# Kernel tuning notes

Hardware: AMD Instinct MI355X
Metric: run time of the kernel (lower is better)

## Reference

```python
import jax, jax.numpy as jnp
import numpy as np

EPS = 1e-5

def _patches(x, k, stride, pad):
    # x: [B, C, H, W] -> [B, L, C*k*k] with patch features ordered (c, kh, kw)
    # matching torch unfold / adder2d weight layout [Cout, Cin, kh, kw].
    B, C, H, W = x.shape
    xp = jnp.pad(x, ((0, 0), (0, 0), (pad, pad), (pad, pad)))
    Ho = (H + 2 * pad - k) // stride + 1
    Wo = (W + 2 * pad - k) // stride + 1
    cols = [xp[:, :, i:i + stride * Ho:stride, j:j + stride * Wo:stride]
            for i in range(k) for j in range(k)]
    p = jnp.stack(cols, axis=2)                      # [B, C, k*k, Ho, Wo]
    p = p.reshape(B, C * k * k, Ho * Wo)             # [B, K, L]
    return p.transpose(0, 2, 1), Ho, Wo              # [B, L, K]


def adder2d(x, w, stride, pad):
    # AdderNet layer: out[n,co,h,w] = -sum_{ci,kh,kw} |x_patch - w[co]|
    B = x.shape[0]
    Cout, Cin, k, _ = w.shape
    P, Ho, Wo = _patches(x, k, stride, pad)          # [B, L, K]
    Wf = w.reshape(Cout, Cin * k * k)                # [Cout, K]

    @jax.checkpoint
    def per_out(wrow):                               # wrow: [K]
        return -jnp.sum(jnp.abs(P - wrow), axis=-1)  # [B, L]

    out = jax.lax.map(per_out, Wf)                   # [Cout, B, L]
    return out.transpose(1, 0, 2).reshape(B, Cout, Ho, Wo)


def batchnorm(x, gamma, beta):
    # training-mode BatchNorm2d: batch statistics over (N, H, W)
    mu = jnp.mean(x, axis=(0, 2, 3), keepdims=True)
    var = jnp.var(x, axis=(0, 2, 3), keepdims=True)
    xn = (x - mu) * jax.lax.rsqrt(var + EPS)
    return xn * gamma[None, :, None, None] + beta[None, :, None, None]


def setup_inputs() -> dict:
    key = jax.random.key(0)
    kx, kw1, kw2 = jax.random.split(key, 3)
    B, C, H, W = 32, 64, 32, 32
    return {
        "x": jax.random.normal(kx, (B, C, H, W), dtype=jnp.float32),
        "w1": jax.random.normal(kw1, (C, C, 3, 3), dtype=jnp.float32),
        "g1": jnp.ones((C,), dtype=jnp.float32),
        "b1": jnp.zeros((C,), dtype=jnp.float32),
        "w2": jax.random.normal(kw2, (C, C, 3, 3), dtype=jnp.float32),
        "g2": jnp.ones((C,), dtype=jnp.float32),
        "b2": jnp.zeros((C,), dtype=jnp.float32),
    }


def reference(x, w1, g1, b1, w2, g2, b2):
    out = adder2d(x, w1, stride=1, pad=1)
    out = jax.nn.relu(batchnorm(out, g1, b1))
    out = adder2d(out, w2, stride=1, pad=1)
    out = batchnorm(out, g2, b2)
    return jax.nn.relu(out + x)
```

## Files before the change

### kernel.cpp

```cpp
#include <hip/hip_runtime.h>

#define CH    64
#define HWHW  1024
#define CHW   65536
#define NPIX  32768.0f

#define QS16   4096.0f
#define QB16   32768.5f
#define Q0P    0x80008000u
#define QINV16 2.44140625e-4f

#define PLSTRIDE 496
#define ROWSTR   51
#define NPLANES  4096

#define AS1 __attribute__((address_space(1)))
#define AS3 __attribute__((address_space(3)))

__device__ __forceinline__ unsigned q16(float x) {
  unsigned u = (unsigned)fmaf(x, QS16, QB16);
  return u > 65535u ? 65535u : u;
}
__device__ __forceinline__ unsigned q16pk(float lo, float hi) {
  return q16(lo) | (q16(hi) << 16);
}

__device__ __forceinline__ unsigned sad16(unsigned x, unsigned w, unsigned a) {
  unsigned d;
  asm("v_sad_u16 %0, %1, %2, %3" : "=v"(d) : "v"(x), "v"(w), "v"(a));
  return d;
}

__device__ __forceinline__ void gll16(const unsigned* g, unsigned* l) {
  __builtin_amdgcn_global_load_lds((const AS1 unsigned*)g, (AS3 unsigned*)l, 16, 0, 0);
}

__global__ __launch_bounds__(256) void prep_kernel(
    const float* __restrict__ w1, const float* __restrict__ w2,
    unsigned* __restrict__ wt1, unsigned* __restrict__ wt2,
    float* __restrict__ stats) {
  int j = blockIdx.x * 256 + threadIdx.x;
  if (j < 256) stats[j] = 0.0f;
  if (j < 18432) {
    int colo = j & 3;
    int t = j >> 2;
    int kw = t % 3; t /= 3;
    int kh = t % 3; t /= 3;
    int cp = t & 7; t >>= 3;
    int wv = t & 3; int cog = t >> 2;
    int co  = cog * 4 + colo;
    int cil = wv * 16 + cp * 2;
    int slo = co * 576 + cil * 9 + kh * 3 + kw;
    wt1[j] = q16pk(w1[slo], w1[slo + 9]);
    wt2[j] = q16pk(w2[slo], w2[slo + 9]);
  }
}

__global__ __launch_bounds__(256) void qx_kernel(
    const float* __restrict__ x, unsigned* __restrict__ xq) {
  int idx = blockIdx.x * 256 + threadIdx.x;
  if (idx >= NPLANES * PLSTRIDE) return;
  int pl = idx / PLSTRIDE;
  int j  = idx - pl * PLSTRIDE;
  int p  = pl & 31;
  int rg = (pl >> 5) & 3;
  int n  = pl >> 7;
  int row = j / ROWSTR;
  int ci  = j - row * ROWSTR;
  int col = ci - 1;
  int hr  = rg * 8 - 1 + row;
  unsigned v = Q0P;
  if (ci >= 1 && ci <= 32 && hr >= 0 && hr < 32) {
    const float* px = x + n * CHW + (2 * p) * HWHW + hr * 32 + col;
    v = q16pk(px[0], px[HWHW]);
  }
  xq[idx] = v;
}

__global__ __launch_bounds__(256) void bnq_kernel(
    const float* __restrict__ A, const float* __restrict__ stats,
    const float* __restrict__ g, const float* __restrict__ b,
    unsigned* __restrict__ xq) {
  int idx = blockIdx.x * 256 + threadIdx.x;
  if (idx >= NPLANES * PLSTRIDE) return;
  int pl = idx / PLSTRIDE;
  int j  = idx - pl * PLSTRIDE;
  int p  = pl & 31;
  int rg = (pl >> 5) & 3;
  int n  = pl >> 7;
  int row = j / ROWSTR;
  int ci  = j - row * ROWSTR;
  int col = ci - 1;
  int hr  = rg * 8 - 1 + row;
  unsigned v = Q0P;
  if (ci >= 1 && ci <= 32 && hr >= 0 && hr < 32) {
    int ch0 = 2 * p, ch1 = 2 * p + 1;
    float mu0 = stats[ch0] * (1.0f / NPIX);
    float va0 = fmaf(-mu0, mu0, stats[64 + ch0] * (1.0f / NPIX));
    float rs0 = rsqrtf(va0 + 1e-5f);
    float ga0 = g[ch0] * rs0;
    float be0 = fmaf(-mu0, ga0, b[ch0]);
    float mu1 = stats[ch1] * (1.0f / NPIX);
    float va1 = fmaf(-mu1, mu1, stats[64 + ch1] * (1.0f / NPIX));
    float rs1 = rsqrtf(va1 + 1e-5f);
    float ga1 = g[ch1] * rs1;
    float be1 = fmaf(-mu1, ga1, b[ch1]);
    float v0 = fmaxf(fmaf(A[n * CHW + ch0 * HWHW + hr * 32 + col], ga0, be0), 0.0f);
    float v1 = fmaxf(fmaf(A[n * CHW + ch1 * HWHW + hr * 32 + col], ga1, be1), 0.0f);
    v = q16pk(v0, v1);
  }
  xq[idx] = v;
}

__global__ __launch_bounds__(256, 6) void adder_kernel(
    const unsigned* __restrict__ xq,
    const unsigned* __restrict__ wt,
    float* __restrict__ out,
    float* __restrict__ stats) {
  const int cog  = blockIdx.x;
  const int rg   = blockIdx.y;
  const int n    = blockIdx.z;
  const int tid  = threadIdx.x;
  const int lane = tid & 63;
  const int wv   = __builtin_amdgcn_readfirstlane(tid >> 6);
  const int co0  = cog * 4;
  const int r0   = lane >> 3;
  const int c0   = (lane & 7) * 4;

  __shared__ __align__(16) unsigned lds[5120];
  unsigned* buf0 = lds + wv * 992;
  unsigned* buf1 = buf0 + 496;
  unsigned* wl   = lds + 3968;
  unsigned* red  = lds;

  const char* gpb = (const char*)(xq + (((n * 4 + rg) * 32) + wv * 8) * PLSTRIDE);
  const int lane16 = lane * 16;

  gll16((const unsigned*)(gpb + lane16), buf0);
  gll16((const unsigned*)(gpb + 960 + lane16), buf0 + 240);
  {
    const uint4* wsrc = (const uint4*)(wt + cog * 1152);
    for (int i = tid; i < 288; i += 256) ((uint4*)wl)[i] = wsrc[i];
  }
  __syncthreads();

  unsigned acc[4][4];
#pragma unroll
  for (int co = 0; co < 4; ++co)
#pragma unroll
    for (int j = 0; j < 4; ++j) acc[co][j] = 0u;

#pragma unroll
  for (int cp = 0; cp < 8; ++cp) {
    if (cp < 7) {
      unsigned* nbuf = (cp & 1) ? buf0 : buf1;
      const char* s = gpb + (cp + 1) * (PLSTRIDE * 4);
      gll16((const unsigned*)(s + lane16), nbuf);
      gll16((const unsigned*)(s + 960 + lane16), nbuf + 240);
      asm volatile("s_waitcnt vmcnt(2)" ::: "memory");
    } else {
      asm volatile("s_waitcnt vmcnt(0)" ::: "memory");
    }
    const unsigned* cbuf = (cp & 1) ? buf1 : buf0;
    const unsigned* wpb = wl + wv * 288 + cp * 36;
#pragma unroll
    for (int kh = 0; kh < 3; ++kh) {
      const uint4* wp = (const uint4*)(wpb + kh * 12);
      uint4 wa = wp[0], wb = wp[1], wc = wp[2];
      unsigned w[12] = {wa.x, wa.y, wa.z, wa.w, wb.x, wb.y, wb.z, wb.w,
                        wc.x, wc.y, wc.z, wc.w};
      const unsigned* rp = cbuf + (r0 + kh) * ROWSTR + c0;
      unsigned xv[6];
#pragma unroll
      for (int j = 0; j < 6; ++j) xv[j] = rp[j];
#pragma unroll
      for (int kw = 0; kw < 3; ++kw)
#pragma unroll
        for (int co = 0; co < 4; ++co) {
          unsigned ww = w[kw * 4 + co];
          acc[co][0] = sad16(xv[kw + 0], ww, acc[co][0]);
          acc[co][1] = sad16(xv[kw + 1], ww, acc[co][1]);
          acc[co][2] = sad16(xv[kw + 2], ww, acc[co][2]);
          acc[co][3] = sad16(xv[kw + 3], ww, acc[co][3]);
        }
    }
  }

  __syncthreads();
  if (wv != 0) {
    unsigned* rp = red + (wv - 1) * 1280 + lane * 20;
#pragma unroll
    for (int co = 0; co < 4; ++co) {
      uint4 q = {acc[co][0], acc[co][1], acc[co][2], acc[co][3]};
      *(uint4*)(rp + co * 4) = q;
    }
  }
  __syncthreads();

  if (wv == 0) {
#pragma unroll
    for (int s = 0; s < 3; ++s) {
      const unsigned* rp = red + s * 1280 + lane * 20;
#pragma unroll
      for (int co = 0; co < 4; ++co) {
        uint4 q = *(const uint4*)(rp + co * 4);
        acc[co][0] += q.x; acc[co][1] += q.y; acc[co][2] += q.z; acc[co][3] += q.w;
      }
    }
    const int ob = n * CHW + (rg * 8 + r0) * 32 + c0;
#pragma unroll
    for (int co = 0; co < 4; ++co) {
      float t0 = -(float)acc[co][0] * QINV16;
      float t1 = -(float)acc[co][1] * QINV16;
      float t2 = -(float)acc[co][2] * QINV16;
      float t3 = -(float)acc[co][3] * QINV16;
      *(float4*)(out + ob + (co0 + co) * HWHW) = make_float4(t0, t1, t2, t3);
      float sm = t0 + t1 + t2 + t3;
      float sq = t0 * t0 + t1 * t1 + t2 * t2 + t3 * t3;
#pragma unroll
      for (int m = 1; m < 64; m <<= 1) {
        sm += __shfl_xor(sm, m);
        sq += __shfl_xor(sq, m);
      }
      if (lane == 0) {
        atomicAdd(stats + co0 + co, sm);
        atomicAdd(stats + 64 + co0 + co, sq);
      }
    }
  }
}

__global__ __launch_bounds__(256) void final_kernel(
    const float* __restrict__ Cbuf, const float* __restrict__ stats,
    const float* __restrict__ g, const float* __restrict__ b,
    const float* __restrict__ xres, float* __restrict__ out) {
  int i = blockIdx.x * 256 + threadIdx.x;
  int c = (i >> 8) & 63;
  float mu  = stats[c] * (1.0f / NPIX);
  float var = fmaf(-mu, mu, stats[64 + c] * (1.0f / NPIX));
  float rs  = rsqrtf(var + 1e-5f);
  float ga  = g[c] * rs;
  float be  = fmaf(-mu, ga, b[c]);
  float4 v = ((const float4*)Cbuf)[i];
  float4 xr = ((const float4*)xres)[i];
  v.x = fmaxf(fmaf(v.x, ga, be) + xr.x, 0.0f);
  v.y = fmaxf(fmaf(v.y, ga, be) + xr.y, 0.0f);
  v.z = fmaxf(fmaf(v.z, ga, be) + xr.z, 0.0f);
  v.w = fmaxf(fmaf(v.w, ga, be) + xr.w, 0.0f);
  ((float4*)out)[i] = v;
}

extern "C" void kernel_launch(void* const* d_in, const int* in_sizes, int n_in,
                              void* d_out, int out_size, void* d_ws, size_t ws_size,
                              hipStream_t stream) {
  const float* x  = (const float*)d_in[0];
  const float* w1 = (const float*)d_in[1];
  const float* g1 = (const float*)d_in[2];
  const float* b1 = (const float*)d_in[3];
  const float* w2 = (const float*)d_in[4];
  const float* g2 = (const float*)d_in[5];
  const float* b2 = (const float*)d_in[6];
  float* outp = (float*)d_out;

  float* ws = (float*)d_ws;
  const size_t NEL = 2097152;
  float*    bufA  = ws;
  unsigned* xq    = (unsigned*)(ws + NEL);
  unsigned* wt1   = xq + (size_t)NPLANES * PLSTRIDE;
  unsigned* wt2   = wt1 + 18432;
  float*    stats = (float*)(wt2 + 18432);

  const int QGRID = (NPLANES * PLSTRIDE) / 256;

  prep_kernel<<<72, 256, 0, stream>>>(w1, w2, wt1, wt2, stats);
  qx_kernel<<<QGRID, 256, 0, stream>>>(x, xq);

  dim3 agrid(16, 4, 32);
  adder_kernel<<<agrid, 256, 0, stream>>>(xq, wt1, bufA, stats);
  bnq_kernel<<<QGRID, 256, 0, stream>>>(bufA, stats, g1, b1, xq);
  adder_kernel<<<agrid, 256, 0, stream>>>(xq, wt2, bufA, stats + 128);
  final_kernel<<<2048, 256, 0, stream>>>(bufA, stats + 128, g2, b2, x, outp);
}
```

Measured before the change: 150.5 us.

## Replace LDS-staged input tiles with register double-buffered direct global loads

The adder kernel stops staging input planes and weights in LDS through global_load_lds. Each thread now loads its 3x6 input window as uint4+uint2 vectors straight from global memory into registers, ping-ponging between two register sets across channel-pair planes. Weights are read from global each step. The plane and row strides are padded to 520/52 so the vector loads are 16-byte aligned, and launch bounds drop to 4 waves per SIMD to fit the larger register footprint. This removes LDS traffic and the LDS-load waits, but relies on the L1 cache to absorb the overlapping halo reads, exposes weight-load latency, adds one redundant wraparound prefetch, and lowers occupancy.

```diff
diff --git a/kernel.cpp b/kernel.cpp
--- a/kernel.cpp
+++ b/kernel.cpp
@@ -10,12 +10,9 @@
 #define Q0P    0x80008000u
 #define QINV16 2.44140625e-4f
 
-#define PLSTRIDE 496
-#define ROWSTR   51
+#define PLSTRIDE 520
+#define ROWSTR   52
 #define NPLANES  4096
-
-#define AS1 __attribute__((address_space(1)))
-#define AS3 __attribute__((address_space(3)))
 
 __device__ __forceinline__ unsigned q16(float x) {
   unsigned u = (unsigned)fmaf(x, QS16, QB16);
@@ -29,10 +26,6 @@
   unsigned d;
   asm("v_sad_u16 %0, %1, %2, %3" : "=v"(d) : "v"(x), "v"(w), "v"(a));
   return d;
-}
-
-__device__ __forceinline__ void gll16(const unsigned* g, unsigned* l) {
-  __builtin_amdgcn_global_load_lds((const AS1 unsigned*)g, (AS3 unsigned*)l, 16, 0, 0);
 }
 
 __global__ __launch_bounds__(256) void prep_kernel(
@@ -112,7 +105,7 @@
   xq[idx] = v;
 }
 
-__global__ __launch_bounds__(256, 6) void adder_kernel(
+__global__ __launch_bounds__(256, 4) void adder_kernel(
     const unsigned* __restrict__ xq,
     const unsigned* __restrict__ wt,
     float* __restrict__ out,
@@ -127,22 +120,11 @@
   const int r0   = lane >> 3;
   const int c0   = (lane & 7) * 4;
 
-  __shared__ __align__(16) unsigned lds[5120];
-  unsigned* buf0 = lds + wv * 992;
-  unsigned* buf1 = buf0 + 496;
-  unsigned* wl   = lds + 3968;
-  unsigned* red  = lds;
-
-  const char* gpb = (const char*)(xq + (((n * 4 + rg) * 32) + wv * 8) * PLSTRIDE);
-  const int lane16 = lane * 16;
-
-  gll16((const unsigned*)(gpb + lane16), buf0);
-  gll16((const unsigned*)(gpb + 960 + lane16), buf0 + 240);
-  {
-    const uint4* wsrc = (const uint4*)(wt + cog * 1152);
-    for (int i = tid; i < 288; i += 256) ((uint4*)wl)[i] = wsrc[i];
-  }
-  __syncthreads();
+  __shared__ unsigned red[3][64][20];
+
+  const unsigned* gp = xq + (size_t)(((n * 4 + rg) * 32) + wv * 8) * PLSTRIDE
+                          + r0 * ROWSTR + c0;
+  const unsigned* wp0 = wt + cog * 1152 + wv * 288;
 
   unsigned acc[4][4];
 #pragma unroll
@@ -150,45 +132,68 @@
 #pragma unroll
     for (int j = 0; j < 4; ++j) acc[co][j] = 0u;
 
-#pragma unroll
-  for (int cp = 0; cp < 8; ++cp) {
-    if (cp < 7) {
-      unsigned* nbuf = (cp & 1) ? buf0 : buf1;
-      const char* s = gpb + (cp + 1) * (PLSTRIDE * 4);
-      gll16((const unsigned*)(s + lane16), nbuf);
-      gll16((const unsigned*)(s + 960 + lane16), nbuf + 240);
-      asm volatile("s_waitcnt vmcnt(2)" ::: "memory");
-    } else {
-      asm volatile("s_waitcnt vmcnt(0)" ::: "memory");
-    }
-    const unsigned* cbuf = (cp & 1) ? buf1 : buf0;
-    const unsigned* wpb = wl + wv * 288 + cp * 36;
-#pragma unroll
-    for (int kh = 0; kh < 3; ++kh) {
-      const uint4* wp = (const uint4*)(wpb + kh * 12);
-      uint4 wa = wp[0], wb = wp[1], wc = wp[2];
-      unsigned w[12] = {wa.x, wa.y, wa.z, wa.w, wb.x, wb.y, wb.z, wb.w,
-                        wc.x, wc.y, wc.z, wc.w};
-      const unsigned* rp = cbuf + (r0 + kh) * ROWSTR + c0;
-      unsigned xv[6];
-#pragma unroll
-      for (int j = 0; j < 6; ++j) xv[j] = rp[j];
-#pragma unroll
-      for (int kw = 0; kw < 3; ++kw)
-#pragma unroll
-        for (int co = 0; co < 4; ++co) {
-          unsigned ww = w[kw * 4 + co];
-          acc[co][0] = sad16(xv[kw + 0], ww, acc[co][0]);
-          acc[co][1] = sad16(xv[kw + 1], ww, acc[co][1]);
-          acc[co][2] = sad16(xv[kw + 2], ww, acc[co][2]);
-          acc[co][3] = sad16(xv[kw + 3], ww, acc[co][3]);
-        }
-    }
+  uint4 xA[3], xB[3];
+  uint2 yA[3], yB[3];
+  unsigned wC[36];
+
+#define LOADX(X, Y, cp) do { \
+    const unsigned* _p = gp + (cp) * PLSTRIDE; \
+    X[0] = *(const uint4*)_p;               Y[0] = *(const uint2*)(_p + 4); \
+    X[1] = *(const uint4*)(_p + ROWSTR);    Y[1] = *(const uint2*)(_p + ROWSTR + 4); \
+    X[2] = *(const uint4*)(_p + 2*ROWSTR);  Y[2] = *(const uint2*)(_p + 2*ROWSTR + 4); \
+  } while (0)
+
+#define LOADW(cp) do { \
+    const uint4* _w = (const uint4*)(wp0 + (cp) * 36); \
+    _Pragma("unroll") \
+    for (int _i = 0; _i < 9; ++_i) { \
+      uint4 _q = _w[_i]; \
+      wC[4*_i] = _q.x; wC[4*_i+1] = _q.y; wC[4*_i+2] = _q.z; wC[4*_i+3] = _q.w; \
+    } \
+  } while (0)
+
+#define COMPUTE(X, Y) do { \
+    _Pragma("unroll") \
+    for (int kh = 0; kh < 3; ++kh) { \
+      unsigned xv0 = X[kh].x, xv1 = X[kh].y, xv2 = X[kh].z; \
+      unsigned xv3 = X[kh].w, xv4 = Y[kh].x, xv5 = Y[kh].y; \
+      _Pragma("unroll") \
+      for (int co = 0; co < 4; ++co) { \
+        unsigned w0 = wC[kh*12 + co], w1 = wC[kh*12 + 4 + co], w2 = wC[kh*12 + 8 + co]; \
+        acc[co][0] = sad16(xv0, w0, acc[co][0]); \
+        acc[co][1] = sad16(xv1, w0, acc[co][1]); \
+        acc[co][2] = sad16(xv2, w0, acc[co][2]); \
+        acc[co][3] = sad16(xv3, w0, acc[co][3]); \
+        acc[co][0] = sad16(xv1, w1, acc[co][0]); \
+        acc[co][1] = sad16(xv2, w1, acc[co][1]); \
+        acc[co][2] = sad16(xv3, w1, acc[co][2]); \
+        acc[co][3] = sad16(xv4, w1, acc[co][3]); \
+        acc[co][0] = sad16(xv2, w2, acc[co][0]); \
+        acc[co][1] = sad16(xv3, w2, acc[co][1]); \
+        acc[co][2] = sad16(xv4, w2, acc[co][2]); \
+        acc[co][3] = sad16(xv5, w2, acc[co][3]); \
+      } \
+    } \
+  } while (0)
+
+  LOADX(xA, yA, 0);
+  LOADW(0);
+
+#pragma unroll 1
+  for (int it = 0; it < 4; ++it) {
+    const int p1 = 2 * it + 1;
+    const int p2 = (p1 + 1) & 7;
+    LOADX(xB, yB, p1);
+    COMPUTE(xA, yA);
+    LOADW(p1);
+    LOADX(xA, yA, p2);
+    COMPUTE(xB, yB);
+    LOADW(p2);
   }
 
   __syncthreads();
   if (wv != 0) {
-    unsigned* rp = red + (wv - 1) * 1280 + lane * 20;
+    unsigned* rp = &red[wv - 1][lane][0];
 #pragma unroll
     for (int co = 0; co < 4; ++co) {
       uint4 q = {acc[co][0], acc[co][1], acc[co][2], acc[co][3]};
@@ -200,7 +205,7 @@
   if (wv == 0) {
 #pragma unroll
     for (int s = 0; s < 3; ++s) {
-      const unsigned* rp = red + s * 1280 + lane * 20;
+      const unsigned* rp = &red[s][lane][0];
 #pragma unroll
       for (int co = 0; co < 4; ++co) {
         uint4 q = *(const uint4*)(rp + co * 4);
```

After: 148.2 us. About the same (-1.6%).

## Drop LDS staging in adder kernel, load planes directly, double output channels per block

Applied to the files above, without the earlier changes.

The adder kernel stops staging input planes in LDS through async global-to-LDS copies. Each thread now reads its 3x6 input window straight from global memory as vector loads, using a padded row stride of 52 so those loads stay aligned. Weights are read directly from global memory, and each block computes 8 output channels instead of 4, which halves the grid and doubles the reuse of each input load. The cost is more registers (the occupancy hint drops from 6 to 4 waves), no cp-loop unrolling, and reliance on the cache instead of explicit prefetch overlap.

```diff
diff --git a/kernel.cpp b/kernel.cpp
--- a/kernel.cpp
+++ b/kernel.cpp
@@ -10,12 +10,9 @@
 #define Q0P    0x80008000u
 #define QINV16 2.44140625e-4f
 
-#define PLSTRIDE 496
-#define ROWSTR   51
+#define PLSTRIDE 520
+#define ROWSTR   52
 #define NPLANES  4096
-
-#define AS1 __attribute__((address_space(1)))
-#define AS3 __attribute__((address_space(3)))
 
 __device__ __forceinline__ unsigned q16(float x) {
   unsigned u = (unsigned)fmaf(x, QS16, QB16);
@@ -29,10 +26,6 @@
   unsigned d;
   asm("v_sad_u16 %0, %1, %2, %3" : "=v"(d) : "v"(x), "v"(w), "v"(a));
   return d;
-}
-
-__device__ __forceinline__ void gll16(const unsigned* g, unsigned* l) {
-  __builtin_amdgcn_global_load_lds((const AS1 unsigned*)g, (AS3 unsigned*)l, 16, 0, 0);
 }
 
 __global__ __launch_bounds__(256) void prep_kernel(
@@ -42,13 +35,13 @@
   int j = blockIdx.x * 256 + threadIdx.x;
   if (j < 256) stats[j] = 0.0f;
   if (j < 18432) {
-    int colo = j & 3;
-    int t = j >> 2;
+    int colo = j & 7;
+    int t = j >> 3;
     int kw = t % 3; t /= 3;
     int kh = t % 3; t /= 3;
     int cp = t & 7; t >>= 3;
     int wv = t & 3; int cog = t >> 2;
-    int co  = cog * 4 + colo;
+    int co  = cog * 8 + colo;
     int cil = wv * 16 + cp * 2;
     int slo = co * 576 + cil * 9 + kh * 3 + kw;
     wt1[j] = q16pk(w1[slo], w1[slo + 9]);
@@ -112,7 +105,7 @@
   xq[idx] = v;
 }
 
-__global__ __launch_bounds__(256, 6) void adder_kernel(
+__global__ __launch_bounds__(256, 4) void adder_kernel(
     const unsigned* __restrict__ xq,
     const unsigned* __restrict__ wt,
     float* __restrict__ out,
@@ -123,74 +116,70 @@
   const int tid  = threadIdx.x;
   const int lane = tid & 63;
   const int wv   = __builtin_amdgcn_readfirstlane(tid >> 6);
-  const int co0  = cog * 4;
+  const int co0  = cog * 8;
   const int r0   = lane >> 3;
   const int c0   = (lane & 7) * 4;
 
-  __shared__ __align__(16) unsigned lds[5120];
-  unsigned* buf0 = lds + wv * 992;
-  unsigned* buf1 = buf0 + 496;
-  unsigned* wl   = lds + 3968;
-  unsigned* red  = lds;
-
-  const char* gpb = (const char*)(xq + (((n * 4 + rg) * 32) + wv * 8) * PLSTRIDE);
-  const int lane16 = lane * 16;
-
-  gll16((const unsigned*)(gpb + lane16), buf0);
-  gll16((const unsigned*)(gpb + 960 + lane16), buf0 + 240);
-  {
-    const uint4* wsrc = (const uint4*)(wt + cog * 1152);
-    for (int i = tid; i < 288; i += 256) ((uint4*)wl)[i] = wsrc[i];
-  }
-  __syncthreads();
-
-  unsigned acc[4][4];
-#pragma unroll
-  for (int co = 0; co < 4; ++co)
+  __shared__ unsigned red[3][64][32];
+
+  const unsigned* gp = xq + (size_t)(((n * 4 + rg) * 32) + wv * 8) * PLSTRIDE
+                          + r0 * ROWSTR + c0;
+  const unsigned* wp0 = wt + cog * 2304 + wv * 576;
+
+  unsigned acc[8][4];
+#pragma unroll
+  for (int co = 0; co < 8; ++co)
 #pragma unroll
     for (int j = 0; j < 4; ++j) acc[co][j] = 0u;
 
-#pragma unroll
+#pragma unroll 1
   for (int cp = 0; cp < 8; ++cp) {
-    if (cp < 7) {
-      unsigned* nbuf = (cp & 1) ? buf0 : buf1;
-      const char* s = gpb + (cp + 1) * (PLSTRIDE * 4);
-      gll16((const unsigned*)(s + lane16), nbuf);
-      gll16((const unsigned*)(s + 960 + lane16), nbuf + 240);
-      asm volatile("s_waitcnt vmcnt(2)" ::: "memory");
-    } else {
-      asm volatile("s_waitcnt vmcnt(0)" ::: "memory");
-    }
-    const unsigned* cbuf = (cp & 1) ? buf1 : buf0;
-    const unsigned* wpb = wl + wv * 288 + cp * 36;
+    const unsigned* _p = gp + cp * PLSTRIDE;
+    uint4 x0 = *(const uint4*)_p;
+    uint2 y0 = *(const uint2*)(_p + 4);
+    uint4 x1 = *(const uint4*)(_p + ROWSTR);
+    uint2 y1 = *(const uint2*)(_p + ROWSTR + 4);
+    uint4 x2 = *(const uint4*)(_p + 2 * ROWSTR);
+    uint2 y2 = *(const uint2*)(_p + 2 * ROWSTR + 4);
+    const unsigned* wpp = wp0 + cp * 72;
+
 #pragma unroll
     for (int kh = 0; kh < 3; ++kh) {
-      const uint4* wp = (const uint4*)(wpb + kh * 12);
-      uint4 wa = wp[0], wb = wp[1], wc = wp[2];
-      unsigned w[12] = {wa.x, wa.y, wa.z, wa.w, wb.x, wb.y, wb.z, wb.w,
-                        wc.x, wc.y, wc.z, wc.w};
-      const unsigned* rp = cbuf + (r0 + kh) * ROWSTR + c0;
-      unsigned xv[6];
-#pragma unroll
-      for (int j = 0; j < 6; ++j) xv[j] = rp[j];
-#pragma unroll
-      for (int kw = 0; kw < 3; ++kw)
-#pragma unroll
-        for (int co = 0; co < 4; ++co) {
-          unsigned ww = w[kw * 4 + co];
-          acc[co][0] = sad16(xv[kw + 0], ww, acc[co][0]);
-          acc[co][1] = sad16(xv[kw + 1], ww, acc[co][1]);
-          acc[co][2] = sad16(xv[kw + 2], ww, acc[co][2]);
-          acc[co][3] = sad16(xv[kw + 3], ww, acc[co][3]);
-        }
+      const uint4* _w = (const uint4*)(wpp + kh * 24);
+      unsigned w[24];
+#pragma unroll
+      for (int i = 0; i < 6; ++i) {
+        uint4 q = _w[i];
+        w[4*i] = q.x; w[4*i+1] = q.y; w[4*i+2] = q.z; w[4*i+3] = q.w;
+      }
+      unsigned xv0, xv1, xv2, xv3, xv4, xv5;
+      if (kh == 0)      { xv0=x0.x; xv1=x0.y; xv2=x0.z; xv3=x0.w; xv4=y0.x; xv5=y0.y; }
+      else if (kh == 1) { xv0=x1.x; xv1=x1.y; xv2=x1.z; xv3=x1.w; xv4=y1.x; xv5=y1.y; }
+      else              { xv0=x2.x; xv1=x2.y; xv2=x2.z; xv3=x2.w; xv4=y2.x; xv5=y2.y; }
+#pragma unroll
+      for (int co = 0; co < 8; ++co) {
+        unsigned w0 = w[co], w1 = w[8 + co], w2 = w[16 + co];
+        acc[co][0] = sad16(xv0, w0, acc[co][0]);
+        acc[co][1] = sad16(xv1, w0, acc[co][1]);
+        acc[co][2] = sad16(xv2, w0, acc[co][2]);
+        acc[co][3] = sad16(xv3, w0, acc[co][3]);
+        acc[co][0] = sad16(xv1, w1, acc[co][0]);
+        acc[co][1] = sad16(xv2, w1, acc[co][1]);
+        acc[co][2] = sad16(xv3, w1, acc[co][2]);
+        acc[co][3] = sad16(xv4, w1, acc[co][3]);
+        acc[co][0] = sad16(xv2, w2, acc[co][0]);
+        acc[co][1] = sad16(xv3, w2, acc[co][1]);
+        acc[co][2] = sad16(xv4, w2, acc[co][2]);
+        acc[co][3] = sad16(xv5, w2, acc[co][3]);
+      }
     }
   }
 
   __syncthreads();
   if (wv != 0) {
-    unsigned* rp = red + (wv - 1) * 1280 + lane * 20;
-#pragma unroll
-    for (int co = 0; co < 4; ++co) {
+    unsigned* rp = &red[wv - 1][lane][0];
+#pragma unroll
+    for (int co = 0; co < 8; ++co) {
       uint4 q = {acc[co][0], acc[co][1], acc[co][2], acc[co][3]};
       *(uint4*)(rp + co * 4) = q;
     }
@@ -200,16 +189,16 @@
   if (wv == 0) {
 #pragma unroll
     for (int s = 0; s < 3; ++s) {
-      const unsigned* rp = red + s * 1280 + lane * 20;
-#pragma unroll
-      for (int co = 0; co < 4; ++co) {
+      const unsigned* rp = &red[s][lane][0];
+#pragma unroll
+      for (int co = 0; co < 8; ++co) {
         uint4 q = *(const uint4*)(rp + co * 4);
         acc[co][0] += q.x; acc[co][1] += q.y; acc[co][2] += q.z; acc[co][3] += q.w;
       }
     }
     const int ob = n * CHW + (rg * 8 + r0) * 32 + c0;
 #pragma unroll
-    for (int co = 0; co < 4; ++co) {
+    for (int co = 0; co < 8; ++co) {
       float t0 = -(float)acc[co][0] * QINV16;
       float t1 = -(float)acc[co][1] * QINV16;
       float t2 = -(float)acc[co][2] * QINV16;
@@ -275,7 +264,7 @@
   prep_kernel<<<72, 256, 0, stream>>>(w1, w2, wt1, wt2, stats);
   qx_kernel<<<QGRID, 256, 0, stream>>>(x, xq);
 
-  dim3 agrid(16, 4, 32);
+  dim3 agrid(8, 4, 32);
   adder_kernel<<<agrid, 256, 0, stream>>>(xq, wt1, bufA, stats);
   bnq_kernel<<<QGRID, 256, 0, stream>>>(bufA, stats, g1, b1, xq);
   adder_kernel<<<agrid, 256, 0, stream>>>(xq, wt2, bufA, stats + 128);
```

After: 171.8 us. 1.14x slower.
